# Performance work log

Measured on AMD Instinct MI355X. Metric: run time of the kernel, lower is better.

The kernel has to match this reference:

```python
import jax, jax.numpy as jnp
import numpy as np

HIDDEN = 1024
HEADS = 16
HEAD = HIDDEN // HEADS
B, S = 4, 2048


def setup_inputs() -> dict:
    key = jax.random.key(0)
    ks = jax.random.split(key, 12)
    sc = 1.0 / np.sqrt(HIDDEN)
    return {
        "query": jax.random.normal(ks[0], (B, S, HIDDEN), jnp.float32),
        "key_in": jax.random.normal(ks[1], (B, S, HIDDEN), jnp.float32),
        "value": jax.random.normal(ks[2], (B, S, HIDDEN), jnp.float32),
        "mask": jax.random.randint(ks[3], (B, S, S), 0, 2, jnp.int32),
        "w_q": jax.random.uniform(ks[4], (HIDDEN, HIDDEN), jnp.float32, -sc, sc),
        "b_q": jax.random.uniform(ks[5], (HIDDEN,), jnp.float32, -sc, sc),
        "w_k": jax.random.uniform(ks[6], (HIDDEN, HIDDEN), jnp.float32, -sc, sc),
        "b_k": jax.random.uniform(ks[7], (HIDDEN,), jnp.float32, -sc, sc),
        "w_v": jax.random.uniform(ks[8], (HIDDEN, HIDDEN), jnp.float32, -sc, sc),
        "b_v": jax.random.uniform(ks[9], (HIDDEN,), jnp.float32, -sc, sc),
    }


def _split_heads(x):
    # [B, S, H*D] -> [B, H, S, D]
    b, s, _ = x.shape
    return x.reshape(b, s, HEADS, HEAD).transpose(0, 2, 1, 3)


def reference(query, key_in, value, mask, w_q, b_q, w_k, b_k, w_v, b_v):
    # torch Linear: x @ W.T + b
    Q = _split_heads(query @ w_q.T + b_q)
    K = _split_heads(key_in @ w_k.T + b_k)
    V = _split_heads(value @ w_v.T + b_v)
    scale = 1.0 / np.sqrt(HEAD).astype(np.float32)
    scores = jnp.einsum("bhqd,bhkd->bhqk", Q, K) * scale
    # mask broadcast over heads; masked_fill where mask == 0
    scores = jnp.where(mask[:, None, :, :] == 0, jnp.float32(-1e9), scores)
    attn = jax.nn.softmax(scores, axis=-1)
    ctx = jnp.einsum("bhqk,bhkd->bhqd", attn, V)
    ctx = ctx.transpose(0, 2, 1, 3).reshape(query.shape[0], -1, HIDDEN)
    return (ctx, attn)
```

## Files before the change

kernel.cpp:

```cpp
#include <hip/hip_runtime.h>
#include <hip/hip_bf16.h>
#include <cstdint>
#include <cstddef>

typedef __attribute__((ext_vector_type(4)))  float f32x4;
typedef __attribute__((ext_vector_type(8)))  short s16x8;
typedef __attribute__((ext_vector_type(8)))  unsigned short u16x8;
typedef __attribute__((ext_vector_type(4)))  unsigned short u16x4;
typedef unsigned short ushort_t;
typedef unsigned long long u64;

#define MFMA_BF16(a, b, c) __builtin_amdgcn_mfma_f32_16x16x32_bf16((a), (b), (c), 0, 0, 0)

constexpr int BATCH  = 4;
constexpr int SEQ    = 2048;
constexpr int NHEAD  = 16;
constexpr int HEADD  = 64;
constexpr int HID    = 1024;
constexpr int BH     = BATCH * NHEAD;
constexpr int MROWS  = BATCH * SEQ;

#define QSCALE 0.180336880091961f

__device__ __forceinline__ ushort_t f2bf(float f) {
  return __builtin_bit_cast(ushort_t, __float2bfloat16(f));
}

__device__ __forceinline__ int ps_off(int q, int k) {
  return q * 136 + ((((k >> 3) ^ ((q >> 3) & 7)) & 15) << 3) + (k & 7);
}

__device__ __forceinline__ void gl2lds16(const ushort_t* g, ushort_t* l) {
  __builtin_amdgcn_global_load_lds(
      (const __attribute__((address_space(1))) void*)g,
      (__attribute__((address_space(3))) void*)l, 16, 0, 0);
}

__global__ __launch_bounds__(256) void prepack_kernel(
    const float* __restrict__ q_in, const float* __restrict__ k_in,
    const float* __restrict__ v_in,
    const float* __restrict__ w_q, const float* __restrict__ w_k,
    const float* __restrict__ w_v,
    ushort_t* __restrict__ Xb, ushort_t* __restrict__ Wb,
    const int* __restrict__ mask, u64* __restrict__ pm) {
  const int z = blockIdx.z;
  if (z == 3) {
    const int nwords = BATCH * SEQ * SEQ / 64;
    const int lane = threadIdx.x & 63;
    int wid = blockIdx.x * 4 + (threadIdx.x >> 6);
    const int step = gridDim.x * 4;
    for (; wid < nwords; wid += step) {
      int mv = __builtin_nontemporal_load(mask + (size_t)wid * 64 + lane);
      u64 bits = __ballot(mv != 0);
      if (lane == 0) pm[wid] = bits;
    }
    return;
  }
  const float* srcX = (z == 0) ? q_in : (z == 1) ? k_in : v_in;
  const float* srcW = (z == 0) ? w_q : (z == 1) ? w_k : w_v;
  ushort_t* dstX = Xb + (size_t)z * MROWS * HID;
  ushort_t* dstW = Wb + (size_t)z * HID * HID;

  const int tid = blockIdx.x * 256 + threadIdx.x;
  const int stride = gridDim.x * 256;

  for (int u = tid; u < MROWS * HID / 8; u += stride) {
    const float* s = srcX + (size_t)u * 8;
    f32x4 a = __builtin_nontemporal_load((const f32x4*)s);
    f32x4 b = __builtin_nontemporal_load((const f32x4*)(s + 4));
    u16x8 o = {f2bf(a[0]), f2bf(a[1]), f2bf(a[2]), f2bf(a[3]),
               f2bf(b[0]), f2bf(b[1]), f2bf(b[2]), f2bf(b[3])};
    __builtin_nontemporal_store(o, (u16x8*)(dstX + (size_t)u * 8));
  }
  for (int u = tid; u < HID * HID / 8; u += stride) {
    const float* s = srcW + (size_t)u * 8;
    f32x4 a = __builtin_nontemporal_load((const f32x4*)s);
    f32x4 b = __builtin_nontemporal_load((const f32x4*)(s + 4));
    u16x8 o = {f2bf(a[0]), f2bf(a[1]), f2bf(a[2]), f2bf(a[3]),
               f2bf(b[0]), f2bf(b[1]), f2bf(b[2]), f2bf(b[3])};
    __builtin_nontemporal_store(o, (u16x8*)(dstW + (size_t)u * 8));
  }
}

__global__ __launch_bounds__(256, 4) void proj_gemm_kernel(
    const ushort_t* __restrict__ Xb, const ushort_t* __restrict__ Wb,
    const float* __restrict__ b_q, const float* __restrict__ b_k,
    const float* __restrict__ b_v,
    ushort_t* __restrict__ Qp, ushort_t* __restrict__ Kp,
    ushort_t* __restrict__ Vp) {
  __shared__ ushort_t As[128 * 64];
  __shared__ ushort_t Bs[128 * 64];

  const int z = blockIdx.z;
  const float* bias = (z == 0) ? b_q : (z == 1) ? b_k : b_v;
  const float scale = (z == 0) ? QSCALE : 1.0f;

  const int tid  = threadIdx.x;
  const int lane = tid & 63;
  const int wave = tid >> 6;
  const int wr = wave >> 1, wc = wave & 1;
  const int lo = lane & 15, hi = lane >> 4;
  const int mb = blockIdx.y, nb = blockIdx.x;

  const ushort_t* Ag = Xb + (size_t)z * MROWS * HID + (size_t)mb * 128 * HID;
  const ushort_t* Bg = Wb + (size_t)z * HID * HID + (size_t)nb * 128 * HID;
  const int lrow = lane >> 3, lcol = (lane & 7) * 8;

  f32x4 acc[4][4];
#pragma unroll
  for (int i = 0; i < 4; i++)
#pragma unroll
    for (int j = 0; j < 4; j++) acc[i][j] = (f32x4){0.f, 0.f, 0.f, 0.f};

  for (int k0 = 0; k0 < HID; k0 += 64) {
#pragma unroll
    for (int it = 0; it < 4; it++) {
      const int r0 = (it * 4 + wave) * 8;
      gl2lds16(Ag + (size_t)(r0 + lrow) * HID + k0 + lcol, &As[(it * 4 + wave) * 512]);
      gl2lds16(Bg + (size_t)(r0 + lrow) * HID + k0 + lcol, &Bs[(it * 4 + wave) * 512]);
    }
    __syncthreads();
#pragma unroll
    for (int kk = 0; kk < 2; kk++) {
      const int ko = kk * 32 + hi * 8;
      s16x8 af[4], bf[4];
#pragma unroll
      for (int i = 0; i < 4; i++)
        af[i] = *(const s16x8*)(&As[(wr * 64 + i * 16 + lo) * 64 + ko]);
#pragma unroll
      for (int j = 0; j < 4; j++)
        bf[j] = *(const s16x8*)(&Bs[(wc * 64 + j * 16 + lo) * 64 + ko]);
#pragma unroll
      for (int i = 0; i < 4; i++)
#pragma unroll
        for (int j = 0; j < 4; j++)
          acc[i][j] = MFMA_BF16(af[i], bf[j], acc[i][j]);
    }
    __syncthreads();
  }

  if (z != 2) {
    ushort_t* out = (z == 0) ? Qp : Kp;
#pragma unroll
    for (int j = 0; j < 4; j++) {
      const int n = nb * 128 + wc * 64 + j * 16 + lo;
      const float bvn = bias[n];
      const int h = n >> 6, d = n & 63;
#pragma unroll
      for (int i = 0; i < 4; i++) {
        const int m0 = mb * 128 + wr * 64 + i * 16 + hi * 4;
#pragma unroll
        for (int r = 0; r < 4; r++) {
          const int m = m0 + r;
          const int b = m >> 11, s = m & 2047;
          float v = (acc[i][j][r] + bvn) * scale;
          __builtin_nontemporal_store(
              f2bf(v), Qp == out ? (out + (((size_t)(b * NHEAD + h) * SEQ) + s) * HEADD + d)
                                 : (out + (((size_t)(b * NHEAD + h) * SEQ) + s) * HEADD + d));
        }
      }
    }
  } else {
#pragma unroll
    for (int j = 0; j < 4; j++) {
      const int n = nb * 128 + wc * 64 + j * 16 + lo;
      const float bvn = bias[n];
      const int h = n >> 6, d = n & 63;
#pragma unroll
      for (int i = 0; i < 4; i++) {
        const int m0 = mb * 128 + wr * 64 + i * 16 + hi * 4;
        const int b = m0 >> 11, s0 = m0 & 2047;
        u16x4 pk = {f2bf(acc[i][j][0] + bvn), f2bf(acc[i][j][1] + bvn),
                    f2bf(acc[i][j][2] + bvn), f2bf(acc[i][j][3] + bvn)};
        __builtin_nontemporal_store(
            pk, (u16x4*)(Vp + ((size_t)(b * NHEAD + h) * HEADD + d) * SEQ + s0));
      }
    }
  }
}

__global__ __launch_bounds__(256, 2) void fused_attn_kernel(
    const ushort_t* __restrict__ Qp, const ushort_t* __restrict__ Kp,
    const ushort_t* __restrict__ Vtg, const u64* __restrict__ pm,
    float* __restrict__ attn, float* __restrict__ ctx) {
  extern __shared__ ushort_t smem[];
  ushort_t* Vt = smem;
  ushort_t* Ps = smem + 8704;

  const int tid  = threadIdx.x;
  const int lane = tid & 63, wave = tid >> 6;
  const int lo = lane & 15, hi = lane >> 4;

  const int f   = blockIdx.x;
  const int xcd = f & 7, i5 = f >> 3;
  const int bh  = xcd * 8 + (i5 & 7);
  const int qb  = i5 >> 3;
  const int b = bh >> 4, h = bh & 15;

  const ushort_t* Qg = Qp + ((size_t)bh * SEQ + qb * 128 + wave * 32) * HEADD;
  s16x8 aq[2][2];
#pragma unroll
  for (int i = 0; i < 2; i++)
#pragma unroll
    for (int kk = 0; kk < 2; kk++)
      aq[i][kk] = *(const s16x8*)(Qg + (size_t)(i * 16 + lo) * HEADD + kk * 32 + hi * 8);

  const ushort_t* Kg = Kp + (size_t)bh * SEQ * HEADD;
  const ushort_t* Vg = Vtg + (size_t)bh * HEADD * SEQ;
  const u64* pmb = pm + (size_t)b * SEQ * 32;
  const int q0 = qb * 128 + wave * 32;

  float lrun[2][4];
#pragma unroll
  for (int i = 0; i < 2; i++)
#pragma unroll
    for (int r = 0; r < 4; r++) lrun[i][r] = 0.f;
  f32x4 pacc[2][4];
#pragma unroll
  for (int i = 0; i < 2; i++)
#pragma unroll
    for (int jd = 0; jd < 4; jd++) pacc[i][jd] = (f32x4){0.f, 0.f, 0.f, 0.f};

  const int vr16 = tid >> 4;
  const int vc8  = (tid & 15) * 8;

  for (int kt = 0; kt < SEQ / 128; kt++) {
    u16x8 vreg[4];
#pragma unroll
    for (int it = 0; it < 4; it++)
      vreg[it] = *(const u16x8*)(Vg + (size_t)(it * 16 + vr16) * SEQ + kt * 128 + vc8);

    f32x4 sacc[2][8];
#pragma unroll
    for (int i = 0; i < 2; i++)
#pragma unroll
      for (int j = 0; j < 8; j++) sacc[i][j] = (f32x4){0.f, 0.f, 0.f, 0.f};
#pragma unroll
    for (int j = 0; j < 8; j++) {
      const ushort_t* kr = Kg + (size_t)(kt * 128 + j * 16 + lo) * HEADD + hi * 8;
      s16x8 b0 = *(const s16x8*)(kr);
      s16x8 b1 = *(const s16x8*)(kr + 32);
      sacc[0][j] = MFMA_BF16(aq[0][0], b0, sacc[0][j]);
      sacc[1][j] = MFMA_BF16(aq[1][0], b0, sacc[1][j]);
      sacc[0][j] = MFMA_BF16(aq[0][1], b1, sacc[0][j]);
      sacc[1][j] = MFMA_BF16(aq[1][1], b1, sacc[1][j]);
    }

#pragma unroll
    for (int it = 0; it < 4; it++)
      *(u16x8*)(&Vt[(it * 16 + vr16) * 136 + vc8]) = vreg[it];

#pragma unroll
    for (int i = 0; i < 2; i++)
#pragma unroll
      for (int r = 0; r < 4; r++) {
        const int q = q0 + i * 16 + hi * 4 + r;
        const u64* pw = pmb + (size_t)q * 32 + kt * 2;
        u64 s0 = pw[0] >> lo, s1 = pw[1] >> lo;
        const int prow = wave * 32 + i * 16 + hi * 4 + r;
        float tsum = 0.f;
#pragma unroll
        for (int j = 0; j < 8; j++) {
          unsigned bit = (unsigned)((j < 4 ? (s0 >> (j * 16)) : (s1 >> ((j - 4) * 16))) & 1ull);
          float s = bit ? sacc[i][j][r] : -1e30f;
          float ev = __builtin_amdgcn_exp2f(s);
          tsum += ev;
          Ps[ps_off(prow, j * 16 + lo)] = f2bf(ev);
        }
        lrun[i][r] += tsum;
      }
    __syncthreads();

#pragma unroll
    for (int kkp = 0; kkp < 4; kkp++) {
      const int ko = kkp * 32 + hi * 8;
      s16x8 ap0 = *(const s16x8*)(&Ps[ps_off(wave * 32 + lo, ko)]);
      s16x8 ap1 = *(const s16x8*)(&Ps[ps_off(wave * 32 + 16 + lo, ko)]);
#pragma unroll
      for (int jd = 0; jd < 4; jd++) {
        s16x8 bv = *(const s16x8*)(&Vt[(jd * 16 + lo) * 136 + ko]);
        pacc[0][jd] = MFMA_BF16(ap0, bv, pacc[0][jd]);
        pacc[1][jd] = MFMA_BF16(ap1, bv, pacc[1][jd]);
      }
    }
    __syncthreads();
  }

  float il[2][4], mi[2][4];
#pragma unroll
  for (int i = 0; i < 2; i++)
#pragma unroll
    for (int r = 0; r < 4; r++) {
      float l = lrun[i][r];
#pragma unroll
      for (int off = 1; off < 16; off <<= 1) l += __shfl_xor(l, off);
      il[i][r] = 1.0f / l;
      mi[i][r] = __builtin_amdgcn_logf(l);
    }
#pragma unroll
  for (int i = 0; i < 2; i++)
#pragma unroll
    for (int jd = 0; jd < 4; jd++)
#pragma unroll
      for (int r = 0; r < 4; r++) {
        const int q = q0 + i * 16 + hi * 4 + r;
        __builtin_nontemporal_store(
            pacc[i][jd][r] * il[i][r],
            ctx + ((size_t)b * SEQ + q) * HID + h * HEADD + jd * 16 + lo);
      }

  for (int kt = 0; kt < SEQ / 128; kt++) {
    f32x4 sacc[2][8];
#pragma unroll
    for (int i = 0; i < 2; i++)
#pragma unroll
      for (int j = 0; j < 8; j++) sacc[i][j] = (f32x4){0.f, 0.f, 0.f, 0.f};
#pragma unroll
    for (int j = 0; j < 8; j++) {
      const ushort_t* kr = Kg + (size_t)(kt * 128 + j * 16 + lo) * HEADD + hi * 8;
      s16x8 b0 = *(const s16x8*)(kr);
      s16x8 b1 = *(const s16x8*)(kr + 32);
      sacc[0][j] = MFMA_BF16(aq[0][0], b0, sacc[0][j]);
      sacc[1][j] = MFMA_BF16(aq[1][0], b0, sacc[1][j]);
      sacc[0][j] = MFMA_BF16(aq[0][1], b1, sacc[0][j]);
      sacc[1][j] = MFMA_BF16(aq[1][1], b1, sacc[1][j]);
    }
#pragma unroll
    for (int i = 0; i < 2; i++)
#pragma unroll
      for (int r = 0; r < 4; r++) {
        const int q = q0 + i * 16 + hi * 4 + r;
        const u64* pw = pmb + (size_t)q * 32 + kt * 2;
        u64 s0 = pw[0] >> lo, s1 = pw[1] >> lo;
        const size_t abase = ((size_t)bh * SEQ + q) * SEQ + (size_t)kt * 128;
        const float miv = mi[i][r];
#pragma unroll
        for (int j = 0; j < 8; j++) {
          unsigned bit = (unsigned)((j < 4 ? (s0 >> (j * 16)) : (s1 >> ((j - 4) * 16))) & 1ull);
          float s = bit ? sacc[i][j][r] : -1e30f;
          __builtin_nontemporal_store(__builtin_amdgcn_exp2f(s - miv),
                                      attn + abase + j * 16 + lo);
        }
      }
  }
}

extern "C" void kernel_launch(void* const* d_in, const int* in_sizes, int n_in,
                              void* d_out, int out_size, void* d_ws, size_t ws_size,
                              hipStream_t stream) {
  const float* query  = (const float*)d_in[0];
  const float* key_in = (const float*)d_in[1];
  const float* value  = (const float*)d_in[2];
  const int*   mask   = (const int*)d_in[3];
  const float* w_q = (const float*)d_in[4];
  const float* b_q = (const float*)d_in[5];
  const float* w_k = (const float*)d_in[6];
  const float* b_k = (const float*)d_in[7];
  const float* w_v = (const float*)d_in[8];
  const float* b_v = (const float*)d_in[9];

  char* ws = (char*)d_ws;
  const size_t proj_elems = (size_t)BATCH * NHEAD * SEQ * HEADD;
  ushort_t* Qp = (ushort_t*)ws;
  ushort_t* Kp = Qp + proj_elems;
  ushort_t* Vp = Kp + proj_elems;
  u64* pmask   = (u64*)(ws + 3 * proj_elems * sizeof(ushort_t));

  float* ctx  = (float*)d_out;
  float* attn = ctx + (size_t)BATCH * SEQ * HID;

  ushort_t* Xb = (ushort_t*)attn;
  ushort_t* Wb = Xb + (size_t)3 * MROWS * HID;

  prepack_kernel<<<dim3(512, 1, 4), dim3(256), 0, stream>>>(
      query, key_in, value, w_q, w_k, w_v, Xb, Wb, mask, pmask);

  proj_gemm_kernel<<<dim3(HID / 128, MROWS / 128, 3), dim3(256), 0, stream>>>(
      Xb, Wb, b_q, b_k, b_v, Qp, Kp, Vp);

  const size_t lds_attn = (8704 + 17408) * sizeof(ushort_t);
  fused_attn_kernel<<<dim3(BH * (SEQ / 128)), dim3(256), lds_attn, stream>>>(
      Qp, Kp, Vp, pmask, attn, ctx);
}
```

Baseline: 679.7 us.

## Recompute attention probabilities with 32x32 MFMA tiles and wider coalesced stores

The second pass, which recomputes scores and writes the normalized attention matrix, now uses 32x32x16 bf16 MFMA instructions over 32-key chunks instead of 16x16x32 tiles over 128-key chunks. Each lane writes 32 contiguous floats per row rather than 16, and per-row log-sum values are shared through a small LDS array after a block barrier. Masked entries are set to zero with a select after the exp instead of feeding -1e30 into the exp. The goal is fewer instructions per output element and better-shaped stores for the dominant attention write, at the cost of one extra barrier and more mask-word loads per chunk.

```diff
diff --git a/kernel.cpp b/kernel.cpp
--- a/kernel.cpp
+++ b/kernel.cpp
@@ -4,13 +4,15 @@
 #include <cstddef>
 
 typedef __attribute__((ext_vector_type(4)))  float f32x4;
+typedef __attribute__((ext_vector_type(16))) float f32x16;
 typedef __attribute__((ext_vector_type(8)))  short s16x8;
 typedef __attribute__((ext_vector_type(8)))  unsigned short u16x8;
 typedef __attribute__((ext_vector_type(4)))  unsigned short u16x4;
 typedef unsigned short ushort_t;
 typedef unsigned long long u64;
 
-#define MFMA_BF16(a, b, c) __builtin_amdgcn_mfma_f32_16x16x32_bf16((a), (b), (c), 0, 0, 0)
+#define MFMA_BF16(a, b, c)   __builtin_amdgcn_mfma_f32_16x16x32_bf16((a), (b), (c), 0, 0, 0)
+#define MFMA32_BF16(a, b, c) __builtin_amdgcn_mfma_f32_32x32x16_bf16((a), (b), (c), 0, 0, 0)
 
 constexpr int BATCH  = 4;
 constexpr int SEQ    = 2048;
@@ -155,8 +157,7 @@
           const int b = m >> 11, s = m & 2047;
           float v = (acc[i][j][r] + bvn) * scale;
           __builtin_nontemporal_store(
-              f2bf(v), Qp == out ? (out + (((size_t)(b * NHEAD + h) * SEQ) + s) * HEADD + d)
-                                 : (out + (((size_t)(b * NHEAD + h) * SEQ) + s) * HEADD + d));
+              f2bf(v), out + (((size_t)(b * NHEAD + h) * SEQ) + s) * HEADD + d);
         }
       }
     }
@@ -186,6 +187,7 @@
   extern __shared__ ushort_t smem[];
   ushort_t* Vt = smem;
   ushort_t* Ps = smem + 8704;
+  __shared__ float mi_sh[128];
 
   const int tid  = threadIdx.x;
   const int lane = tid & 63, wave = tid >> 6;
@@ -286,7 +288,7 @@
     __syncthreads();
   }
 
-  float il[2][4], mi[2][4];
+  float il[2][4];
 #pragma unroll
   for (int i = 0; i < 2; i++)
 #pragma unroll
@@ -295,7 +297,8 @@
 #pragma unroll
       for (int off = 1; off < 16; off <<= 1) l += __shfl_xor(l, off);
       il[i][r] = 1.0f / l;
-      mi[i][r] = __builtin_amdgcn_logf(l);
+      if (lo == 0)
+        mi_sh[wave * 32 + i * 16 + hi * 4 + r] = __builtin_amdgcn_logf(l);
     }
 #pragma unroll
   for (int i = 0; i < 2; i++)
@@ -308,40 +311,47 @@
             pacc[i][jd][r] * il[i][r],
             ctx + ((size_t)b * SEQ + q) * HID + h * HEADD + jd * 16 + lo);
       }
-
-  for (int kt = 0; kt < SEQ / 128; kt++) {
-    f32x4 sacc[2][8];
-#pragma unroll
-    for (int i = 0; i < 2; i++)
-#pragma unroll
-      for (int j = 0; j < 8; j++) sacc[i][j] = (f32x4){0.f, 0.f, 0.f, 0.f};
-#pragma unroll
-    for (int j = 0; j < 8; j++) {
-      const ushort_t* kr = Kg + (size_t)(kt * 128 + j * 16 + lo) * HEADD + hi * 8;
-      s16x8 b0 = *(const s16x8*)(kr);
-      s16x8 b1 = *(const s16x8*)(kr + 32);
-      sacc[0][j] = MFMA_BF16(aq[0][0], b0, sacc[0][j]);
-      sacc[1][j] = MFMA_BF16(aq[1][0], b0, sacc[1][j]);
-      sacc[0][j] = MFMA_BF16(aq[0][1], b1, sacc[0][j]);
-      sacc[1][j] = MFMA_BF16(aq[1][1], b1, sacc[1][j]);
-    }
-#pragma unroll
-    for (int i = 0; i < 2; i++)
-#pragma unroll
-      for (int r = 0; r < 4; r++) {
-        const int q = q0 + i * 16 + hi * 4 + r;
-        const u64* pw = pmb + (size_t)q * 32 + kt * 2;
-        u64 s0 = pw[0] >> lo, s1 = pw[1] >> lo;
-        const size_t abase = ((size_t)bh * SEQ + q) * SEQ + (size_t)kt * 128;
-        const float miv = mi[i][r];
-#pragma unroll
-        for (int j = 0; j < 8; j++) {
-          unsigned bit = (unsigned)((j < 4 ? (s0 >> (j * 16)) : (s1 >> ((j - 4) * 16))) & 1ull);
-          float s = bit ? sacc[i][j][r] : -1e30f;
-          __builtin_nontemporal_store(__builtin_amdgcn_exp2f(s - miv),
-                                      attn + abase + j * 16 + lo);
-        }
-      }
+  __syncthreads();
+
+  const int l31 = lane & 31, h32 = lane >> 5;
+  const int q0w = qb * 128 + wave * 32;
+  const ushort_t* Qg32 = Qp + (size_t)bh * SEQ * HEADD;
+
+  s16x8 aq32[4];
+#pragma unroll
+  for (int mf = 0; mf < 4; mf++)
+    aq32[mf] = *(const s16x8*)(Qg32 + (size_t)(q0w + l31) * HEADD + mf * 16 + h32 * 8);
+
+  int qr[16];
+  float mi32[16];
+#pragma unroll
+  for (int r = 0; r < 16; r++) {
+    const int row = (r & 3) + 8 * (r >> 2) + 4 * h32;
+    qr[r]   = q0w + row;
+    mi32[r] = mi_sh[wave * 32 + row];
+  }
+  const unsigned* pm32 = (const unsigned*)pmb;
+  float* ab = attn + (size_t)bh * SEQ * SEQ;
+
+  for (int kc = 0; kc < SEQ / 32; kc++) {
+    s16x8 bk[4];
+#pragma unroll
+    for (int mf = 0; mf < 4; mf++)
+      bk[mf] = *(const s16x8*)(Kg + (size_t)(kc * 32 + l31) * HEADD + mf * 16 + h32 * 8);
+    f32x16 sacc;
+#pragma unroll
+    for (int t = 0; t < 16; t++) sacc[t] = 0.f;
+    sacc = MFMA32_BF16(aq32[0], bk[0], sacc);
+    sacc = MFMA32_BF16(aq32[1], bk[1], sacc);
+    sacc = MFMA32_BF16(aq32[2], bk[2], sacc);
+    sacc = MFMA32_BF16(aq32[3], bk[3], sacc);
+#pragma unroll
+    for (int r = 0; r < 16; r++) {
+      unsigned mw = pm32[(size_t)qr[r] * 64 + kc];
+      float e = __builtin_amdgcn_exp2f(sacc[r] - mi32[r]);
+      e = ((mw >> l31) & 1u) ? e : 0.f;
+      __builtin_nontemporal_store(e, ab + (size_t)qr[r] * SEQ + kc * 32 + l31);
+    }
   }
 }
 
```

New measurement: 709.4 us. 4.4% more time.

## Split fused attention into PV kernel and separate attention-probability store kernel

Applied to the files above, without the earlier changes.

The single fused attention kernel, which computed context and then recomputed scores to write the full attention matrix, is split into two kernels. The first computes context and writes per-row log-sum-exp to a workspace buffer. The second recomputes QK scores and stores normalized probabilities without LDS, so it can run at higher occupancy. Launch bounds are raised to allow more blocks per CU, at the cost of an extra launch and a small global round trip for the row statistics.

```diff
diff --git a/kernel.cpp b/kernel.cpp
--- a/kernel.cpp
+++ b/kernel.cpp
@@ -155,8 +155,7 @@
           const int b = m >> 11, s = m & 2047;
           float v = (acc[i][j][r] + bvn) * scale;
           __builtin_nontemporal_store(
-              f2bf(v), Qp == out ? (out + (((size_t)(b * NHEAD + h) * SEQ) + s) * HEADD + d)
-                                 : (out + (((size_t)(b * NHEAD + h) * SEQ) + s) * HEADD + d));
+              f2bf(v), out + (((size_t)(b * NHEAD + h) * SEQ) + s) * HEADD + d);
         }
       }
     }
@@ -179,10 +178,10 @@
   }
 }
 
-__global__ __launch_bounds__(256, 2) void fused_attn_kernel(
+__global__ __launch_bounds__(256, 3) void attn_pv_kernel(
     const ushort_t* __restrict__ Qp, const ushort_t* __restrict__ Kp,
     const ushort_t* __restrict__ Vtg, const u64* __restrict__ pm,
-    float* __restrict__ attn, float* __restrict__ ctx) {
+    float* __restrict__ mi_ws, float* __restrict__ ctx) {
   extern __shared__ ushort_t smem[];
   ushort_t* Vt = smem;
   ushort_t* Ps = smem + 8704;
@@ -286,7 +285,7 @@
     __syncthreads();
   }
 
-  float il[2][4], mi[2][4];
+  float il[2][4];
 #pragma unroll
   for (int i = 0; i < 2; i++)
 #pragma unroll
@@ -295,7 +294,8 @@
 #pragma unroll
       for (int off = 1; off < 16; off <<= 1) l += __shfl_xor(l, off);
       il[i][r] = 1.0f / l;
-      mi[i][r] = __builtin_amdgcn_logf(l);
+      if (lo == 0)
+        mi_ws[bh * SEQ + q0 + i * 16 + hi * 4 + r] = __builtin_amdgcn_logf(l);
     }
 #pragma unroll
   for (int i = 0; i < 2; i++)
@@ -308,6 +308,40 @@
             pacc[i][jd][r] * il[i][r],
             ctx + ((size_t)b * SEQ + q) * HID + h * HEADD + jd * 16 + lo);
       }
+}
+
+__global__ __launch_bounds__(256, 4) void attn_store_kernel(
+    const ushort_t* __restrict__ Qp, const ushort_t* __restrict__ Kp,
+    const u64* __restrict__ pm, const float* __restrict__ mi_ws,
+    float* __restrict__ attn) {
+  const int tid  = threadIdx.x;
+  const int lane = tid & 63, wave = tid >> 6;
+  const int lo = lane & 15, hi = lane >> 4;
+
+  const int f   = blockIdx.x;
+  const int xcd = f & 7, i5 = f >> 3;
+  const int bh  = xcd * 8 + (i5 & 7);
+  const int qb  = i5 >> 3;
+  const int b = bh >> 4;
+
+  const ushort_t* Qg = Qp + ((size_t)bh * SEQ + qb * 128 + wave * 32) * HEADD;
+  s16x8 aq[2][2];
+#pragma unroll
+  for (int i = 0; i < 2; i++)
+#pragma unroll
+    for (int kk = 0; kk < 2; kk++)
+      aq[i][kk] = *(const s16x8*)(Qg + (size_t)(i * 16 + lo) * HEADD + kk * 32 + hi * 8);
+
+  const ushort_t* Kg = Kp + (size_t)bh * SEQ * HEADD;
+  const u64* pmb = pm + (size_t)b * SEQ * 32;
+  const int q0 = qb * 128 + wave * 32;
+
+  float mi[2][4];
+#pragma unroll
+  for (int i = 0; i < 2; i++)
+#pragma unroll
+    for (int r = 0; r < 4; r++)
+      mi[i][r] = mi_ws[bh * SEQ + q0 + i * 16 + hi * 4 + r];
 
   for (int kt = 0; kt < SEQ / 128; kt++) {
     f32x4 sacc[2][8];
@@ -365,6 +399,7 @@
   ushort_t* Kp = Qp + proj_elems;
   ushort_t* Vp = Kp + proj_elems;
   u64* pmask   = (u64*)(ws + 3 * proj_elems * sizeof(ushort_t));
+  float* mi_ws = (float*)(pmask + (size_t)BATCH * SEQ * SEQ / 64);
 
   float* ctx  = (float*)d_out;
   float* attn = ctx + (size_t)BATCH * SEQ * HID;
@@ -378,7 +413,10 @@
   proj_gemm_kernel<<<dim3(HID / 128, MROWS / 128, 3), dim3(256), 0, stream>>>(
       Xb, Wb, b_q, b_k, b_v, Qp, Kp, Vp);
 
-  const size_t lds_attn = (8704 + 17408) * sizeof(ushort_t);
-  fused_attn_kernel<<<dim3(BH * (SEQ / 128)), dim3(256), lds_attn, stream>>>(
-      Qp, Kp, Vp, pmask, attn, ctx);
-}
+  const size_t lds_pv = (8704 + 17408) * sizeof(ushort_t);
+  attn_pv_kernel<<<dim3(BH * (SEQ / 128)), dim3(256), lds_pv, stream>>>(
+      Qp, Kp, Vp, pmask, mi_ws, ctx);
+
+  attn_store_kernel<<<dim3(BH * (SEQ / 128)), dim3(256), 0, stream>>>(
+      Qp, Kp, pmask, mi_ws, attn);
+}
```

Result: slower. 786.0 us (+15.6%).
